# Kernel optimization log

Measured on AMD Instinct MI355X. Metric: run time of the kernel, lower is better.

The kernel has to match this reference:

```python
import jax
import jax.numpy as jnp
import numpy as np

D_MODEL = 768
D_STATE = 64
D_CONV = 4
EXPAND = 2
D_INNER = D_MODEL * EXPAND  # 1536
BATCH = 2
SEQ = 1024


def setup_inputs() -> dict:
    key = jax.random.key(0)
    ks = jax.random.split(key, 8)
    s = 0.02
    return {
        "x": jax.random.normal(ks[0], (BATCH, SEQ, D_MODEL), jnp.float32),
        "W_in": jax.random.normal(ks[1], (2 * D_INNER, D_MODEL), jnp.float32) * s,
        "conv_w": jax.random.normal(ks[2], (D_INNER, 1, D_CONV), jnp.float32) * 0.3,
        "conv_b": jnp.zeros((D_INNER,), jnp.float32),
        "W_x": jax.random.normal(ks[3], (2 * D_STATE + 1, D_INNER), jnp.float32) * s,
        "dt_w": jax.random.normal(ks[4], (D_INNER, 1), jnp.float32),
        "dt_b": jax.random.normal(ks[5], (D_INNER,), jnp.float32) * 0.1,
        "A_log": jnp.log(jnp.arange(1, D_STATE + 1, dtype=jnp.float32)),
        "D_param": jnp.ones((D_INNER,), jnp.float32),
        "W_out": jax.random.normal(ks[6], (D_MODEL, D_INNER), jnp.float32) * s,
    }


def reference(x, W_in, conv_w, conv_b, W_x, dt_w, dt_b, A_log, D_param, W_out):
    B, L, _ = x.shape
    # in_proj: [B,L,2*d_inner], split into ssm branch and gate z
    xz = jnp.einsum('bld,ed->ble', x, W_in)
    x_p, z = jnp.split(xz, 2, axis=-1)
    # depthwise causal conv1d (pad=d_conv-1 on the left, truncated to seq_len)
    pad = jnp.pad(x_p, ((0, 0), (D_CONV - 1, 0), (0, 0)))
    x_conv = conv_b + sum(pad[:, i:i + L, :] * conv_w[:, 0, i] for i in range(D_CONV))
    x_conv = jax.nn.silu(x_conv)
    # x_proj -> dt(1), B(d_state), C(d_state)
    x_dbl = jnp.einsum('bld,ed->ble', x_conv, W_x)
    dt_in = x_dbl[..., :1]                      # [B,L,1]
    Bm = x_dbl[..., 1:1 + D_STATE]              # [B,L,N]
    Cm = x_dbl[..., 1 + D_STATE:]               # [B,L,N]
    # dt_proj: Linear(1, d_inner) + softplus -> [B,L,d_inner]
    dt = jax.nn.softplus(dt_in * dt_w[:, 0] + dt_b)
    A = -jnp.exp(A_log)                          # [N]

    def step(h, ts):
        dt_t, B_t, C_t, xc_t = ts                # [B,d], [B,N], [B,N], [B,d]
        dA = jnp.exp(dt_t[:, :, None] * A)       # [B,d,N]
        dB = dt_t[:, :, None] * B_t[:, None, :]  # [B,d,N]
        h = h * dA + dB * xc_t[:, :, None]       # [B,d,N]
        y = jnp.einsum('bdn,bn->bd', h, C_t) + D_param * xc_t
        return h, y

    h0 = jnp.zeros((B, D_INNER, D_STATE), x.dtype)
    ts = tuple(jnp.moveaxis(a, 1, 0) for a in (dt, Bm, Cm, x_conv))
    _, ys = jax.lax.scan(step, h0, ts)           # ys: [L,B,d]
    y = jnp.moveaxis(ys, 0, 1) * jax.nn.silu(z)
    return jnp.einsum('bld,ed->ble', y, W_out)
```

## Files before the change

### kernel.cpp

```cpp
#include <hip/hip_runtime.h>
#include <hip/hip_bf16.h>
#include <stdint.h>

typedef __hip_bfloat16 bf16;
typedef __attribute__((ext_vector_type(8))) short short8;
typedef __attribute__((ext_vector_type(4))) short short4v;
typedef __attribute__((ext_vector_type(4))) float floatx4;

#define D_MODEL 768
#define D_STATE 64
#define D_INNER 1536
#define BATCH   2
#define SEQ     1024
#define M_TOK   (BATCH * SEQ)
#define CH      32
#define CHUNK   64
#define NCHUNK  (SEQ / CHUNK)

static __device__ __forceinline__ float bf2f(bf16 v) { return __bfloat162float(v); }

__global__ __launch_bounds__(256) void cvt_all(
    const float* __restrict__ x, const float* __restrict__ Win,
    const float* __restrict__ Wx1, const float* __restrict__ Wout,
    bf16* __restrict__ xbf, bf16* __restrict__ winbf,
    bf16* __restrict__ wxbf, bf16* __restrict__ woutbf)
{
  const int i = blockIdx.x * 256 + threadIdx.x;
  const float* s; bf16* dst; int off;
  if (i < 393216)       { s = x;    dst = xbf;    off = i; }
  else if (i < 983040)  { s = Win;  dst = winbf;  off = i - 393216; }
  else if (i < 1032192) { s = Wx1;  dst = wxbf;   off = i - 983040; }
  else                  { s = Wout; dst = woutbf; off = i - 1032192; }
  const float4 v = ((const float4*)s)[off];
  short4v o;
  o.x = (short)__bfloat16_as_ushort(__float2bfloat16(v.x));
  o.y = (short)__bfloat16_as_ushort(__float2bfloat16(v.y));
  o.z = (short)__bfloat16_as_ushort(__float2bfloat16(v.z));
  o.w = (short)__bfloat16_as_ushort(__float2bfloat16(v.w));
  ((short4v*)dst)[off] = o;
}

template <int BM, int BN, int SPLITK, typename OutT>
__global__ __launch_bounds__(256) void gemm_bt(
    const bf16* __restrict__ A, const bf16* __restrict__ B,
    OutT* __restrict__ C, int M, int N, int K)
{
  __shared__ __align__(16) short As[BM * 32];
  __shared__ __align__(16) short Bs[BN * 32];
  constexpr int WM = BM / 2, WN = BN / 2;
  constexpr int IM = WM / 16, JN = WN / 16;
  constexpr int LA = BM / 64, LB = BN / 64;
  const int tid  = threadIdx.x;
  const int lane = tid & 63;
  const int quad = lane >> 4;
  const int l15  = lane & 15;
  const int wv   = tid >> 6;
  const int wm   = (wv >> 1) * WM;
  const int wn   = (wv & 1) * WN;
  const long m0  = (long)blockIdx.y * BM;
  const long n0  = (long)blockIdx.x * BN;
  const int kpb  = K / SPLITK;
  const int kbeg = blockIdx.z * kpb;
  const int kend = kbeg + kpb;

  floatx4 acc[IM][JN];
#pragma unroll
  for (int i = 0; i < IM; ++i)
#pragma unroll
    for (int j = 0; j < JN; ++j)
      acc[i][j] = (floatx4){0.f, 0.f, 0.f, 0.f};

  for (int kt = kbeg; kt < kend; kt += 32) {
    __syncthreads();
#pragma unroll
    for (int i = 0; i < LA; ++i) {
      const int f  = tid + (i << 8);
      const int fm = f >> 2;
      const int fk = (f & 3) << 3;
      const bf16* ga = A + (m0 + fm) * (long)K + kt + fk;
      __builtin_amdgcn_global_load_lds(
          (const __attribute__((address_space(1))) uint32_t*)ga,
          (__attribute__((address_space(3))) uint32_t*)&As[f << 3], 16, 0, 0);
    }
#pragma unroll
    for (int i = 0; i < LB; ++i) {
      const int f  = tid + (i << 8);
      const int fm = f >> 2;
      const int fk = (f & 3) << 3;
      const bf16* gb = B + (n0 + fm) * (long)K + kt + fk;
      __builtin_amdgcn_global_load_lds(
          (const __attribute__((address_space(1))) uint32_t*)gb,
          (__attribute__((address_space(3))) uint32_t*)&Bs[f << 3], 16, 0, 0);
    }
    __syncthreads();
    short8 af[IM], bf_[JN];
#pragma unroll
    for (int i = 0; i < IM; ++i)
      af[i]  = *(const short8*)&As[(wm + i * 16 + l15) * 32 + (quad << 3)];
#pragma unroll
    for (int j = 0; j < JN; ++j)
      bf_[j] = *(const short8*)&Bs[(wn + j * 16 + l15) * 32 + (quad << 3)];
#pragma unroll
    for (int i = 0; i < IM; ++i)
#pragma unroll
      for (int j = 0; j < JN; ++j)
        acc[i][j] = __builtin_amdgcn_mfma_f32_16x16x32_bf16(af[i], bf_[j], acc[i][j], 0, 0, 0);
  }

#pragma unroll
  for (int i = 0; i < IM; ++i)
#pragma unroll
    for (int j = 0; j < JN; ++j)
#pragma unroll
      for (int r = 0; r < 4; ++r) {
        const long gm = m0 + wm + i * 16 + quad * 4 + r;
        const long gn = n0 + wn + j * 16 + l15;
        const float v = acc[i][j][r];
        if constexpr (SPLITK > 1)
          atomicAdd((float*)&C[gm * N + gn], v);
        else if constexpr (sizeof(OutT) == 2)
          C[gm * N + gn] = __float2bfloat16(v);
        else
          C[gm * N + gn] = v;
      }
}

__global__ __launch_bounds__(256) void conv_silu(
    const bf16* __restrict__ xz, const float* __restrict__ conv_w,
    const float* __restrict__ conv_b, const float* __restrict__ Wx0,
    bf16* __restrict__ xconv, bf16* __restrict__ zsilu,
    float* __restrict__ dtin)
{
  const int idx = blockIdx.x * 256 + threadIdx.x;
  const int d = idx % D_INNER;
  const int m = idx / D_INNER;
  const int l = m & (SEQ - 1);
  float acc = conv_b[d];
#pragma unroll
  for (int i = 0; i < 4; ++i) {
    const int lp = l + i - 3;
    if (lp >= 0)
      acc = fmaf(bf2f(xz[(long)(m - 3 + i) * 3072 + d]), conv_w[d * 4 + i], acc);
  }
  const float xc = acc / (1.f + __expf(-acc));
  xconv[idx] = __float2bfloat16(xc);
  const float z = bf2f(xz[(long)m * 3072 + D_INNER + d]);
  zsilu[idx] = __float2bfloat16(z / (1.f + __expf(-z)));

  float part = xc * Wx0[d];
#pragma unroll
  for (int off = 32; off > 0; off >>= 1) part += __shfl_xor(part, off, 64);
  __shared__ float red[4];
  if ((threadIdx.x & 63) == 0) red[threadIdx.x >> 6] = part;
  __syncthreads();
  if (threadIdx.x == 0)
    atomicAdd(&dtin[m], red[0] + red[1] + red[2] + red[3]);
}

template <bool FINAL>
__global__ __launch_bounds__(1024, 8) void scan_chunk(
    const float* __restrict__ xdbl, const float* __restrict__ dtin,
    const bf16* __restrict__ xconv, const bf16* __restrict__ zsilu,
    const float* __restrict__ A_log, const float* __restrict__ D_param,
    const float* __restrict__ dt_w, const float* __restrict__ dt_b,
    float* __restrict__ Hbuf, float* __restrict__ Tbuf,
    bf16* __restrict__ ygated)
{
  extern __shared__ __align__(16) char smem[];
  float*  sB  = (float*)smem;
  float*  sC  = (float*)(smem + 8192);
  float4* sp4 = (float4*)(smem + 16384);
  bf16*   sy  = (bf16*)(smem + 49152);
  float2* sp2 = (float2*)(smem + 8192);

  const int tid  = threadIdx.x;
  const int t16  = tid & 15;
  const int dl   = tid >> 4;
  const int dg   = blockIdx.x;
  const int c    = blockIdx.y;
  const int b    = blockIdx.z;
  const int d0   = dg * 64;
  const int n0   = t16 * 4;
  const long mb  = (long)b * SEQ;
  const int c0   = c * CHUNK;

  float An[4];
#pragma unroll
  for (int i = 0; i < 4; ++i) An[i] = -__expf(A_log[n0 + i]);

  float4 pB4; float2 pB2;
  float pdt[2], pxc[2], pzs[2];

  auto ISSUE = [&](int cc) {
    const int row = tid >> 5;
    if constexpr (FINAL) {
      pB4 = ((const float4*)(xdbl + (mb + cc + row) * 128))[tid & 31];
    } else {
      pB2 = ((const float2*)(xdbl + (mb + cc + row) * 128))[tid & 31];
    }
#pragma unroll
    for (int j = 0; j < 2; ++j) {
      const int item = tid + j * 1024;
      const int s = item >> 6, dl2 = item & 63;
      const long m = mb + cc + s;
      pdt[j] = dtin[m];
      pxc[j] = bf2f(xconv[m * D_INNER + d0 + dl2]);
      if constexpr (FINAL) pzs[j] = bf2f(zsilu[m * D_INNER + d0 + dl2]);
    }
  };

  auto COMMIT = [&]() {
    const int row = tid >> 5;
    if constexpr (FINAL) {
      const int col4 = tid & 31;
      if (col4 < 16) *(float4*)&sB[row * 64 + col4 * 4] = pB4;
      else           *(float4*)&sC[row * 64 + (col4 - 16) * 4] = pB4;
    } else {
      *(float2*)&sB[row * 64 + (tid & 31) * 2] = pB2;
    }
#pragma unroll
    for (int j = 0; j < 2; ++j) {
      const int item = tid + j * 1024;
      const int s = item >> 6, dl2 = item & 63;
      const float xv = fmaf(pdt[j], dt_w[d0 + dl2], dt_b[d0 + dl2]);
      const float dtv = fmaxf(xv, 0.f) + __logf(1.f + __expf(-fabsf(xv)));
      if constexpr (FINAL)
        sp4[s * 64 + dl2] = (float4){dtv, dtv * pxc[j], D_param[d0 + dl2] * pxc[j], pzs[j]};
      else
        sp2[s * 64 + dl2] = (float2){dtv, dtv * pxc[j]};
    }
  };

  ISSUE(c0);
  COMMIT();
  __syncthreads();

  const long base = ((long)(b * NCHUNK + c) * D_INNER + d0 + dl) * 64 + n0;
  float h0, h1, h2, h3;
  if constexpr (FINAL) {
    const float4 S = *(const float4*)&Hbuf[base];
    h0 = S.x; h1 = S.y; h2 = S.z; h3 = S.w;
  } else {
    h0 = h1 = h2 = h3 = 0.f;
  }
  float Tsum = 0.f;

  for (int cs = 0; cs < CHUNK; cs += CH) {
    const bool more = (cs + CH < CHUNK);
    if (more) ISSUE(c0 + cs + CH);
#pragma unroll 4
    for (int s = 0; s < CH; ++s) {
      const float4 Bv = *(const float4*)&sB[s * 64 + n0];
      float dtv, q;
      float4 pk;
      if constexpr (FINAL) {
        pk = sp4[s * 64 + dl];
        dtv = pk.x; q = pk.y;
      } else {
        const float2 p2 = sp2[s * 64 + dl];
        dtv = p2.x; q = p2.y;
      }
      const float e0 = __expf(dtv * An[0]);
      const float e1 = __expf(dtv * An[1]);
      const float e2 = __expf(dtv * An[2]);
      const float e3 = __expf(dtv * An[3]);
      h0 = fmaf(h0, e0, q * Bv.x);
      h1 = fmaf(h1, e1, q * Bv.y);
      h2 = fmaf(h2, e2, q * Bv.z);
      h3 = fmaf(h3, e3, q * Bv.w);
      if constexpr (FINAL) {
        const float4 Cv = *(const float4*)&sC[s * 64 + n0];
        float p = fmaf(h3, Cv.w, fmaf(h2, Cv.z, fmaf(h1, Cv.y, h0 * Cv.x)));
        p += __shfl_xor(p, 1, 64);
        p += __shfl_xor(p, 2, 64);
        p += __shfl_xor(p, 4, 64);
        p += __shfl_xor(p, 8, 64);
        if (t16 == 0) sy[s * 64 + dl] = __float2bfloat16((p + pk.z) * pk.w);
      } else {
        Tsum += dtv;
      }
    }
    if constexpr (FINAL) {
      __syncthreads();
      {
        const int row = tid >> 5, col2 = tid & 31;
        const uint32_t v = ((const uint32_t*)sy)[tid];
        *(uint32_t*)&ygated[(mb + c0 + cs + row) * (long)D_INNER + d0 + col2 * 2] = v;
      }
      if (more) { COMMIT(); __syncthreads(); }
    } else {
      if (more) { __syncthreads(); COMMIT(); __syncthreads(); }
    }
  }

  if constexpr (!FINAL) {
    *(float4*)&Hbuf[base] = (float4){h0, h1, h2, h3};
    if (t16 == 0) Tbuf[(b * NCHUNK + c) * D_INNER + d0 + dl] = Tsum;
  }
}

__global__ __launch_bounds__(256) void scan_link(
    float* __restrict__ H, const float* __restrict__ Tbuf,
    const float* __restrict__ A_log)
{
  const int t = blockIdx.x * 256 + threadIdx.x;
  const int b = t / 24576;
  const int r = t % 24576;
  const int d = r >> 4;
  const int n4 = r & 15;
  float An[4];
#pragma unroll
  for (int i = 0; i < 4; ++i) An[i] = -__expf(A_log[n4 * 4 + i]);
  float4* H4 = (float4*)H;
  float4 S = {0.f, 0.f, 0.f, 0.f};
#pragma unroll
  for (int c = 0; c < NCHUNK; ++c) {
    const long i4 = ((long)(b * NCHUNK + c) * D_INNER + d) * 16 + n4;
    const float4 Hc = H4[i4];
    const float T = Tbuf[(b * NCHUNK + c) * D_INNER + d];
    H4[i4] = S;
    S.x = fmaf(__expf(An[0] * T), S.x, Hc.x);
    S.y = fmaf(__expf(An[1] * T), S.y, Hc.y);
    S.z = fmaf(__expf(An[2] * T), S.z, Hc.z);
    S.w = fmaf(__expf(An[3] * T), S.w, Hc.w);
  }
}

extern "C" void kernel_launch(void* const* d_in, const int* in_sizes, int n_in,
                              void* d_out, int out_size, void* d_ws, size_t ws_size,
                              hipStream_t stream)
{
  const float* x       = (const float*)d_in[0];
  const float* W_in    = (const float*)d_in[1];
  const float* conv_w  = (const float*)d_in[2];
  const float* conv_b  = (const float*)d_in[3];
  const float* W_x     = (const float*)d_in[4];
  const float* dt_w    = (const float*)d_in[5];
  const float* dt_b    = (const float*)d_in[6];
  const float* A_log   = (const float*)d_in[7];
  const float* D_param = (const float*)d_in[8];
  const float* W_out   = (const float*)d_in[9];
  float* out = (float*)d_out;

  char* ws = (char*)d_ws;
  bf16*  xzbf   = (bf16*)(ws);
  bf16*  xconv  = (bf16*)(ws + 12582912);
  bf16*  zsilu  = (bf16*)(ws + 18874368);
  float* xdbl   = (float*)(ws + 25165824);
  float* dtin   = (float*)(ws + 26214400);
  float* Tbuf   = (float*)(ws + 26222592);
  float* Hbuf   = (float*)(ws + 26419200);
  bf16*  ygated = (bf16*)(ws + 39002112);
  bf16*  xbf    = (bf16*)(ws + 45293568);
  bf16*  Winbf  = (bf16*)(ws + 48439296);
  bf16*  Wxbf   = (bf16*)(ws + 53157888);
  bf16*  Woutbf = (bf16*)(ws + 53551104);

  hipMemsetAsync(dtin, 0, M_TOK * sizeof(float), stream);
  hipMemsetAsync(xdbl, 0, M_TOK * 128 * sizeof(float), stream);

  cvt_all<<<5184, 256, 0, stream>>>(x, W_in, W_x + D_INNER, W_out,
                                    xbf, Winbf, Wxbf, Woutbf);

  gemm_bt<128, 128, 1, bf16><<<dim3(24, 16), 256, 0, stream>>>(
      xbf, Winbf, xzbf, M_TOK, 2 * D_INNER, D_MODEL);

  conv_silu<<<(M_TOK * D_INNER) / 256, 256, 0, stream>>>(
      xzbf, conv_w, conv_b, W_x, xconv, zsilu, dtin);

  gemm_bt<64, 64, 4, float><<<dim3(2, 32, 4), 256, 0, stream>>>(
      xconv, Wxbf, xdbl, M_TOK, 128, D_INNER);

  scan_chunk<false><<<dim3(24, NCHUNK, 2), 1024, 24576, stream>>>(
      xdbl, dtin, xconv, nullptr, A_log, nullptr, dt_w, dt_b,
      Hbuf, Tbuf, nullptr);
  scan_link<<<192, 256, 0, stream>>>(Hbuf, Tbuf, A_log);
  scan_chunk<true><<<dim3(24, NCHUNK, 2), 1024, 53248, stream>>>(
      xdbl, dtin, xconv, zsilu, A_log, D_param, dt_w, dt_b,
      Hbuf, nullptr, ygated);

  gemm_bt<64, 64, 1, float><<<dim3(12, 32), 256, 0, stream>>>(
      ygated, Woutbf, out, M_TOK, D_MODEL, D_INNER);
}
```

Measured before the change: 266.1 us.

## Vectorize conv_silu by 8 channels, swizzle reductions in scan, merge memsets

The conv_silu kernel now handles 8 channels per thread using 128-bit bf16 loads and stores, with a per-wavefront atomic instead of a shared-memory block reduction. The launch shrinks to 1536 blocks, and each token's 192 threads span several blocks, so dtin receives several atomics per token. In the scan, the inner loop is fully unrolled with hoisted base pointers, and the 16-lane reduction uses ds_swizzle instead of shfl_xor. The two memsets are merged into one because dtin directly follows xdbl in the workspace.

```diff
diff --git a/kernel.cpp b/kernel.cpp
--- a/kernel.cpp
+++ b/kernel.cpp
@@ -18,6 +18,9 @@
 #define NCHUNK  (SEQ / CHUNK)
 
 static __device__ __forceinline__ float bf2f(bf16 v) { return __bfloat162float(v); }
+
+#define SWZ_ADD(p, pat) \
+  p += __uint_as_float(__builtin_amdgcn_ds_swizzle(__float_as_uint(p), pat))
 
 __global__ __launch_bounds__(256) void cvt_all(
     const float* __restrict__ x, const float* __restrict__ Win,
@@ -131,30 +134,65 @@
     bf16* __restrict__ xconv, bf16* __restrict__ zsilu,
     float* __restrict__ dtin)
 {
-  const int idx = blockIdx.x * 256 + threadIdx.x;
-  const int d = idx % D_INNER;
-  const int m = idx / D_INNER;
-  const int l = m & (SEQ - 1);
-  float acc = conv_b[d];
+  const int t = blockIdx.x * 256 + threadIdx.x;
+  const int m  = t / 192;
+  const int d8 = (t % 192) * 8;
+  const int l  = m & (SEQ - 1);
+
+  float acc[8];
+#pragma unroll
+  for (int j = 0; j < 8; j += 4) {
+    const float4 cb = *(const float4*)&conv_b[d8 + j];
+    acc[j] = cb.x; acc[j+1] = cb.y; acc[j+2] = cb.z; acc[j+3] = cb.w;
+  }
+  float4 cw[8];
+#pragma unroll
+  for (int j = 0; j < 8; ++j) cw[j] = ((const float4*)conv_w)[d8 + j];
+
 #pragma unroll
   for (int i = 0; i < 4; ++i) {
-    const int lp = l + i - 3;
-    if (lp >= 0)
-      acc = fmaf(bf2f(xz[(long)(m - 3 + i) * 3072 + d]), conv_w[d * 4 + i], acc);
-  }
-  const float xc = acc / (1.f + __expf(-acc));
-  xconv[idx] = __float2bfloat16(xc);
-  const float z = bf2f(xz[(long)m * 3072 + D_INNER + d]);
-  zsilu[idx] = __float2bfloat16(z / (1.f + __expf(-z)));
-
-  float part = xc * Wx0[d];
+    if (l + i - 3 >= 0) {
+      const short8 row = *(const short8*)&xz[(long)(m - 3 + i) * 3072 + d8];
+#pragma unroll
+      for (int j = 0; j < 8; ++j) {
+        const float xvj = bf2f(__ushort_as_bfloat16((unsigned short)row[j]));
+        const float w = (&cw[j].x)[i];
+        acc[j] = fmaf(xvj, w, acc[j]);
+      }
+    }
+  }
+
+  short8 oxc;
+  float xcv[8];
+#pragma unroll
+  for (int j = 0; j < 8; ++j) {
+    const float xc = acc[j] / (1.f + __expf(-acc[j]));
+    xcv[j] = xc;
+    oxc[j] = (short)__bfloat16_as_ushort(__float2bfloat16(xc));
+  }
+  *(short8*)&xconv[(long)m * D_INNER + d8] = oxc;
+
+  const short8 zrow = *(const short8*)&xz[(long)m * 3072 + D_INNER + d8];
+  short8 ozs;
+#pragma unroll
+  for (int j = 0; j < 8; ++j) {
+    const float z = bf2f(__ushort_as_bfloat16((unsigned short)zrow[j]));
+    ozs[j] = (short)__bfloat16_as_ushort(__float2bfloat16(z / (1.f + __expf(-z))));
+  }
+  *(short8*)&zsilu[(long)m * D_INNER + d8] = ozs;
+
+  float part = 0.f;
+#pragma unroll
+  for (int j = 0; j < 8; j += 4) {
+    const float4 w0 = *(const float4*)&Wx0[d8 + j];
+    part = fmaf(xcv[j], w0.x, part);
+    part = fmaf(xcv[j+1], w0.y, part);
+    part = fmaf(xcv[j+2], w0.z, part);
+    part = fmaf(xcv[j+3], w0.w, part);
+  }
 #pragma unroll
   for (int off = 32; off > 0; off >>= 1) part += __shfl_xor(part, off, 64);
-  __shared__ float red[4];
-  if ((threadIdx.x & 63) == 0) red[threadIdx.x >> 6] = part;
-  __syncthreads();
-  if (threadIdx.x == 0)
-    atomicAdd(&dtin[m], red[0] + red[1] + red[2] + red[3]);
+  if ((threadIdx.x & 63) == 0) atomicAdd(&dtin[m], part);
 }
 
 template <bool FINAL>
@@ -245,19 +283,24 @@
   }
   float Tsum = 0.f;
 
+  const float*  sBb  = sB + n0;
+  const float*  sCb  = sC + n0;
+  const float4* sp4b = sp4 + dl;
+  const float2* sp2b = sp2 + dl;
+
   for (int cs = 0; cs < CHUNK; cs += CH) {
     const bool more = (cs + CH < CHUNK);
     if (more) ISSUE(c0 + cs + CH);
-#pragma unroll 4
+#pragma unroll
     for (int s = 0; s < CH; ++s) {
-      const float4 Bv = *(const float4*)&sB[s * 64 + n0];
+      const float4 Bv = *(const float4*)&sBb[s * 64];
       float dtv, q;
       float4 pk;
       if constexpr (FINAL) {
-        pk = sp4[s * 64 + dl];
+        pk = sp4b[s * 64];
         dtv = pk.x; q = pk.y;
       } else {
-        const float2 p2 = sp2[s * 64 + dl];
+        const float2 p2 = sp2b[s * 64];
         dtv = p2.x; q = p2.y;
       }
       const float e0 = __expf(dtv * An[0]);
@@ -269,12 +312,12 @@
       h2 = fmaf(h2, e2, q * Bv.z);
       h3 = fmaf(h3, e3, q * Bv.w);
       if constexpr (FINAL) {
-        const float4 Cv = *(const float4*)&sC[s * 64 + n0];
+        const float4 Cv = *(const float4*)&sCb[s * 64];
         float p = fmaf(h3, Cv.w, fmaf(h2, Cv.z, fmaf(h1, Cv.y, h0 * Cv.x)));
-        p += __shfl_xor(p, 1, 64);
-        p += __shfl_xor(p, 2, 64);
-        p += __shfl_xor(p, 4, 64);
-        p += __shfl_xor(p, 8, 64);
+        SWZ_ADD(p, 0x041F);
+        SWZ_ADD(p, 0x081F);
+        SWZ_ADD(p, 0x101F);
+        SWZ_ADD(p, 0x201F);
         if (t16 == 0) sy[s * 64 + dl] = __float2bfloat16((p + pk.z) * pk.w);
       } else {
         Tsum += dtv;
@@ -356,8 +399,7 @@
   bf16*  Wxbf   = (bf16*)(ws + 53157888);
   bf16*  Woutbf = (bf16*)(ws + 53551104);
 
-  hipMemsetAsync(dtin, 0, M_TOK * sizeof(float), stream);
-  hipMemsetAsync(xdbl, 0, M_TOK * 128 * sizeof(float), stream);
+  hipMemsetAsync(xdbl, 0, M_TOK * 128 * sizeof(float) + M_TOK * sizeof(float), stream);
 
   cvt_all<<<5184, 256, 0, stream>>>(x, W_in, W_x + D_INNER, W_out,
                                     xbf, Winbf, Wxbf, Woutbf);
@@ -365,7 +407,7 @@
   gemm_bt<128, 128, 1, bf16><<<dim3(24, 16), 256, 0, stream>>>(
       xbf, Winbf, xzbf, M_TOK, 2 * D_INNER, D_MODEL);
 
-  conv_silu<<<(M_TOK * D_INNER) / 256, 256, 0, stream>>>(
+  conv_silu<<<1536, 256, 0, stream>>>(
       xzbf, conv_w, conv_b, W_x, xconv, zsilu, dtin);
 
   gemm_bt<64, 64, 4, float><<<dim3(2, 32, 4), 256, 0, stream>>>(
```

Result: slower. 372.2 us (+39.9%).
